# Optimization experiments

Measured on AMD Instinct MI355X. Metric: run time of the kernel, lower is better.

The kernel has to match this reference:

```python
import jax, jax.numpy as jnp
import numpy as np

D_MODEL = 1024
N_HEADS = 16
D_K = D_MODEL // N_HEADS


def setup_inputs() -> dict:
    key = jax.random.key(0)
    ks = jax.random.split(key, 11)
    B, S = 2, 2048
    scale = 1.0 / np.sqrt(D_MODEL)
    inp = {
        "Q_in": jax.random.normal(ks[0], (B, S, D_MODEL), jnp.float32),
        "K_in": jax.random.normal(ks[1], (B, S, D_MODEL), jnp.float32),
        "V_in": jax.random.normal(ks[2], (B, S, D_MODEL), jnp.float32),
        # torch nn.Linear convention: y = x @ W.T + b, W shape [out, in]
        "W_q": jax.random.normal(ks[3], (D_MODEL, D_MODEL), jnp.float32) * scale,
        "b_q": jax.random.normal(ks[4], (D_MODEL,), jnp.float32) * scale,
        "W_k": jax.random.normal(ks[5], (D_MODEL, D_MODEL), jnp.float32) * scale,
        "b_k": jax.random.normal(ks[6], (D_MODEL,), jnp.float32) * scale,
        "W_v": jax.random.normal(ks[7], (D_MODEL, D_MODEL), jnp.float32) * scale,
        "b_v": jax.random.normal(ks[8], (D_MODEL,), jnp.float32) * scale,
        "W_o": jax.random.normal(ks[9], (D_MODEL, D_MODEL), jnp.float32) * scale,
        "b_o": jax.random.normal(ks[10], (D_MODEL,), jnp.float32) * scale,
    }
    return inp


def reference(Q_in, K_in, V_in, W_q, b_q, W_k, b_k, W_v, b_v, W_o, b_o):
    B, S, _ = Q_in.shape

    def proj(x, W, b):
        # [B,S,D] -> [B,H,S,dk]
        y = x @ W.T + b
        return y.reshape(B, S, N_HEADS, D_K).transpose(0, 2, 1, 3)

    Q = proj(Q_in, W_q, b_q)
    K = proj(K_in, W_k, b_k)
    V = proj(V_in, W_v, b_v)

    scores = jnp.einsum("bhqd,bhkd->bhqk", Q, K) / jnp.sqrt(jnp.float32(D_K))
    attn_weights = jax.nn.softmax(scores, axis=-1)
    ctx = jnp.einsum("bhqk,bhkd->bhqd", attn_weights, V)
    ctx = ctx.transpose(0, 2, 1, 3).reshape(B, S, D_MODEL)
    output = ctx @ W_o.T + b_o
    return output, attn_weights
```

## Files before the change

kernel.cpp:

```cpp
#include <hip/hip_runtime.h>
#include <hip/hip_bf16.h>
#include <stdint.h>

typedef __attribute__((ext_vector_type(8))) short short8;
typedef __attribute__((ext_vector_type(4))) short short4v;
typedef __attribute__((ext_vector_type(4))) float f32x4;
typedef __attribute__((ext_vector_type(2))) float f32x2;

#define MFMA16x16x32(A, B, C) __builtin_amdgcn_mfma_f32_16x16x32_bf16((A), (B), (C), 0, 0, 0)

static constexpr int kS  = 2048;
static constexpr int kD  = 1024;
static constexpr int kDK = 64;

static constexpr size_t OFF_XQ  = 0;
static constexpr size_t OFF_XK  = 4194304;
static constexpr size_t OFF_XV  = 8388608;
static constexpr size_t OFF_W   = 12582912;
static constexpr size_t OFF_QP  = 16777216;
static constexpr size_t OFF_KP  = 20971520;
static constexpr size_t OFF_VT  = 25165824;
static constexpr size_t OFF_CTX = 29360128;

__device__ __forceinline__ short f2bf(float f) {
  __hip_bfloat16 h = __float2bfloat16(f);
  return *reinterpret_cast<short*>(&h);
}

__global__ __launch_bounds__(256) void cvt_kernel(
    const float* __restrict__ xq, const float* __restrict__ xk, const float* __restrict__ xv,
    const float* __restrict__ wq, const float* __restrict__ wk, const float* __restrict__ wv,
    const float* __restrict__ wo, __hip_bfloat16* __restrict__ dst)
{
  int g = blockIdx.x * 256 + threadIdx.x;
  const float* src;
  __hip_bfloat16* d;
  int rel;
  if (g < 3145728) {
    int seg = g >> 20; rel = g & 1048575;
    src = seg == 0 ? xq : (seg == 1 ? xk : xv);
    d = dst + (size_t)seg * 4194304;
  } else {
    int g2 = g - 3145728; int seg = g2 >> 18; rel = g2 & 262143;
    src = seg == 0 ? wq : (seg == 1 ? wk : (seg == 2 ? wv : wo));
    d = dst + OFF_W + (size_t)seg * 1048576;
  }
  float4 v = ((const float4*)src)[rel];
  short4v o;
  o.x = f2bf(v.x); o.y = f2bf(v.y); o.z = f2bf(v.z); o.w = f2bf(v.w);
  ((short4v*)d)[rel] = o;
}

__device__ __forceinline__ void stage_tile(short* lds, const __hip_bfloat16* g0, int t) {
  #pragma unroll
  for (int c = 0; c < 2; ++c) {
    const int e = t * 8 + c * 2048;
    const int row = e >> 5;
    const int kk = e & 31;
    __builtin_amdgcn_global_load_lds(
        (const __attribute__((address_space(1))) void*)(g0 + (size_t)row * kD + kk),
        (__attribute__((address_space(3))) void*)(lds + e), 16, 0, 0);
  }
}

__device__ __forceinline__ void gemm_main(const __hip_bfloat16* X, const __hip_bfloat16* W,
                                          short* As, short* Bs, f32x4 acc[4][4])
{
  const int t = threadIdx.x;
  const int lane = t & 63;
  const int wv = t >> 6;
  const int wr = wv >> 1, wc = wv & 1;
  const int fr = lane & 15;
  const int fc = (lane >> 4) * 8;
  for (int k0 = 0; k0 < kD; k0 += 32) {
    stage_tile(As, X + k0, t);
    stage_tile(Bs, W + k0, t);
    __syncthreads();
    short8 af[4], bfv[4];
    #pragma unroll
    for (int i = 0; i < 4; ++i) af[i]  = *(const short8*)&As[(wr * 64 + i * 16 + fr) * 32 + fc];
    #pragma unroll
    for (int i = 0; i < 4; ++i) bfv[i] = *(const short8*)&Bs[(wc * 64 + i * 16 + fr) * 32 + fc];
    #pragma unroll
    for (int i = 0; i < 4; ++i)
      #pragma unroll
      for (int j = 0; j < 4; ++j)
        acc[i][j] = MFMA16x16x32(af[i], bfv[j], acc[i][j]);
    __syncthreads();
  }
}

__global__ __launch_bounds__(256) void qkv_gemm(
    const __hip_bfloat16* __restrict__ Xq, const __hip_bfloat16* __restrict__ Xk,
    const __hip_bfloat16* __restrict__ Xv, const __hip_bfloat16* __restrict__ Wbase,
    const float* __restrict__ bq, const float* __restrict__ bk, const float* __restrict__ bv,
    __hip_bfloat16* __restrict__ Qp, __hip_bfloat16* __restrict__ Kp,
    __hip_bfloat16* __restrict__ Vt)
{
  __shared__ __align__(16) short As[128 * 32];
  __shared__ __align__(16) short Bs[128 * 32];
  const int z  = blockIdx.z;
  const int m0 = blockIdx.y * 128, n0 = blockIdx.x * 128;
  const __hip_bfloat16* X = (z == 0 ? Xq : (z == 1 ? Xk : Xv)) + (size_t)m0 * kD;
  const __hip_bfloat16* W = Wbase + (size_t)z * (kD * kD) + (size_t)n0 * kD;
  const float* bias = (z == 0 ? bq : (z == 1 ? bk : bv));
  f32x4 acc[4][4] = {};
  gemm_main(X, W, As, Bs, acc);

  const int lane = threadIdx.x & 63;
  const int wv = threadIdx.x >> 6;
  const int wr = wv >> 1, wc = wv & 1;
  short* dstQK = (short*)(z == 0 ? Qp : Kp);
  short* dstV  = (short*)Vt;
  #pragma unroll
  for (int i = 0; i < 4; ++i) {
    #pragma unroll
    for (int j = 0; j < 4; ++j) {
      #pragma unroll
      for (int r = 0; r < 4; ++r) {
        int m = m0 + wr * 64 + i * 16 + (lane >> 4) * 4 + r;
        int n = n0 + wc * 64 + j * 16 + (lane & 15);
        float y = acc[i][j][r] + bias[n];
        if (z == 0) y *= 0.125f;
        int b = m >> 11, sq = m & 2047, h = n >> 6, d = n & 63;
        if (z < 2)
          dstQK[((size_t)(b * 16 + h) * kS + sq) * kDK + d] = f2bf(y);
        else
          dstV[((size_t)(b * 16 + h) * kDK + d) * kS + sq] = f2bf(y);
      }
    }
  }
}

__global__ __launch_bounds__(256) void attn_pass1(
    const __hip_bfloat16* __restrict__ Qp, const __hip_bfloat16* __restrict__ Kp,
    const __hip_bfloat16* __restrict__ Vt, __hip_bfloat16* __restrict__ Ctx,
    float* __restrict__ rinvp)
{
  __shared__ __align__(16) short Ks[2][32][68];
  __shared__ __align__(16) short Vs[2][64][36];
  __shared__ __align__(16) short Ps[4][16][36];
  const int t = threadIdx.x;
  const int lane = t & 63;
  const int w = t >> 6;
  const int fr = lane & 15;
  const int g4 = lane >> 4;
  const int fc = g4 * 8;

  const int id  = blockIdx.x;
  const int swz = (id & 7) * 128 + (id >> 3);
  const int bh  = swz >> 5;
  const int q0  = (swz & 31) * 64 + w * 16;

  const __hip_bfloat16* Qh = Qp + (size_t)bh * kS * kDK;
  const __hip_bfloat16* Kh = Kp + (size_t)bh * kS * kDK;
  const __hip_bfloat16* Vh = Vt + (size_t)bh * kDK * kS;

  const short8 qf0 = *(const short8*)(Qh + (size_t)(q0 + fr) * kDK + fc);
  const short8 qf1 = *(const short8*)(Qh + (size_t)(q0 + fr) * kDK + 32 + fc);

  const int kr = t >> 3, kc = (t & 7) * 8;
  const int vr = t >> 2, vc = (t & 3) * 8;

  f32x4 ctxacc[4] = {};
  float ssumq = 0.f;

  short8 kA, vA, kB, vB;

#define LOAD_T(KREG, VREG, TI)                                                   \
  KREG = *(const short8*)(Kh + (size_t)((TI) * 32 + kr) * kDK + kc);             \
  VREG = *(const short8*)(Vh + (size_t)vr * kS + (TI) * 32 + vc);

#define STORE_T(KREG, VREG, BUF)                                                 \
  *(short8*)&Ks[BUF][kr][kc] = KREG;                                             \
  *(short8*)&Vs[BUF][vr][vc] = VREG;

#define COMPUTE_T(BUF)                                                           \
  {                                                                              \
    short8 k0a = *(const short8*)&Ks[BUF][fr][fc];                               \
    short8 k0b = *(const short8*)&Ks[BUF][fr][32 + fc];                          \
    short8 k1a = *(const short8*)&Ks[BUF][16 + fr][fc];                          \
    short8 k1b = *(const short8*)&Ks[BUF][16 + fr][32 + fc];                     \
    f32x4 s0 = {}; s0 = MFMA16x16x32(k0a, qf0, s0); s0 = MFMA16x16x32(k0b, qf1, s0); \
    f32x4 s1 = {}; s1 = MFMA16x16x32(k1a, qf0, s1); s1 = MFMA16x16x32(k1b, qf1, s1); \
    float e00 = __expf(s0[0]), e01 = __expf(s0[1]);                              \
    float e02 = __expf(s0[2]), e03 = __expf(s0[3]);                              \
    float e10 = __expf(s1[0]), e11 = __expf(s1[1]);                              \
    float e12 = __expf(s1[2]), e13 = __expf(s1[3]);                              \
    ssumq += (e00 + e01) + (e02 + e03) + (e10 + e11) + (e12 + e13);              \
    short4v p0, p1;                                                              \
    p0.x = f2bf(e00); p0.y = f2bf(e01); p0.z = f2bf(e02); p0.w = f2bf(e03);      \
    p1.x = f2bf(e10); p1.y = f2bf(e11); p1.z = f2bf(e12); p1.w = f2bf(e13);      \
    *(short4v*)&Ps[w][fr][g4 * 4]      = p0;                                     \
    *(short4v*)&Ps[w][fr][16 + g4 * 4] = p1;                                     \
    short8 pf = *(const short8*)&Ps[w][fr][fc];                                  \
    _Pragma("unroll")                                                            \
    for (int dc = 0; dc < 4; ++dc) {                                             \
      short8 vf = *(const short8*)&Vs[BUF][dc * 16 + fr][fc];                    \
      ctxacc[dc] = MFMA16x16x32(pf, vf, ctxacc[dc]);                             \
    }                                                                            \
  }

  LOAD_T(kA, vA, 0);
  STORE_T(kA, vA, 0);
  LOAD_T(kB, vB, 1);
  __syncthreads();

  for (int i = 0; i < 64; i += 2) {
    COMPUTE_T(0);
    STORE_T(kB, vB, 1);
    if (i + 2 < 64) { LOAD_T(kA, vA, i + 2); }
    __syncthreads();
    COMPUTE_T(1);
    if (i + 2 < 64) { STORE_T(kA, vA, 0); }
    if (i + 3 < 64) { LOAD_T(kB, vB, i + 3); }
    __syncthreads();
  }

  float s = ssumq;
  s += __shfl_xor(s, 16);
  s += __shfl_xor(s, 32);
  const float rvq = 1.0f / s;
  if (g4 == 0) rinvp[(size_t)bh * kS + q0 + fr] = rvq;

  float rinv4[4];
  #pragma unroll
  for (int j = 0; j < 4; ++j) rinv4[j] = __shfl(rvq, g4 * 4 + j, 16);

  const int b = bh >> 4, h = bh & 15;
  #pragma unroll
  for (int dc = 0; dc < 4; ++dc) {
    #pragma unroll
    for (int j = 0; j < 4; ++j) {
      int r = g4 * 4 + j;
      float v = ctxacc[dc][j] * rinv4[j];
      ((short*)Ctx)[((size_t)(b * kS + q0 + r)) * kD + h * kDK + dc * 16 + fr] = f2bf(v);
    }
  }
#undef LOAD_T
#undef STORE_T
#undef COMPUTE_T
}

__global__ __launch_bounds__(256) void fused_tail(
    const __hip_bfloat16* __restrict__ Ctx, const __hip_bfloat16* __restrict__ Wo,
    const float* __restrict__ bo, float* __restrict__ out,
    const __hip_bfloat16* __restrict__ Qp, const __hip_bfloat16* __restrict__ Kp,
    const float* __restrict__ rinvp, float* __restrict__ Aw)
{
  __shared__ __align__(16) short As[128 * 32];
  __shared__ __align__(16) short Bs[128 * 32];
  const int t = threadIdx.x;
  const int lane = t & 63;
  const int w = t >> 6;
  const int fr = lane & 15;
  const int g4 = lane >> 4;
  const int fc = g4 * 8;

  if (blockIdx.x < 256) {
    const int m0 = (blockIdx.x >> 3) * 128, n0 = (blockIdx.x & 7) * 128;
    f32x4 acc[4][4] = {};
    gemm_main(Ctx + (size_t)m0 * kD, Wo + (size_t)n0 * kD, As, Bs, acc);
    const int wr = w >> 1, wc = w & 1;
    #pragma unroll
    for (int i = 0; i < 4; ++i) {
      #pragma unroll
      for (int j = 0; j < 4; ++j) {
        #pragma unroll
        for (int r = 0; r < 4; ++r) {
          int m = m0 + wr * 64 + i * 16 + g4 * 4 + r;
          int n = n0 + wc * 64 + j * 16 + fr;
          __builtin_nontemporal_store(acc[i][j][r] + bo[n], &out[(size_t)m * kD + n]);
        }
      }
    }
    return;
  }

  const int id  = blockIdx.x - 256;
  const int swz = (id & 7) * 512 + (id >> 3);
  const int bh  = swz >> 7;
  const int ksg = (swz >> 5) & 3;
  const int q0  = (swz & 31) * 64 + w * 16;
  const int k0  = ksg * 512;

  const __hip_bfloat16* Qh = Qp + (size_t)bh * kS * kDK;
  const __hip_bfloat16* Kh = Kp + (size_t)bh * kS * kDK;

  const short8 qf0 = *(const short8*)(Qh + (size_t)(q0 + fr) * kDK + fc);
  const short8 qf1 = *(const short8*)(Qh + (size_t)(q0 + fr) * kDK + 32 + fc);

  const float rvq = rinvp[(size_t)bh * kS + q0 + fr];
  float* aw = Aw + ((size_t)bh * kS + q0 + fr) * kS;

  short8 ka[8], kb[8];

#define LOADK(ARR, KT_)                                                          \
  _Pragma("unroll")                                                              \
  for (int c = 0; c < 4; ++c) {                                                  \
    ARR[2 * c]     = *(const short8*)(Kh + (size_t)((KT_) + c * 16 + fr) * kDK + fc);      \
    ARR[2 * c + 1] = *(const short8*)(Kh + (size_t)((KT_) + c * 16 + fr) * kDK + 32 + fc); \
  }

#define CSTORE(ARR, KT_)                                                         \
  _Pragma("unroll")                                                              \
  for (int c = 0; c < 4; ++c) {                                                  \
    f32x4 st = {};                                                               \
    st = MFMA16x16x32(ARR[2 * c], qf0, st);                                      \
    st = MFMA16x16x32(ARR[2 * c + 1], qf1, st);                                  \
    f32x4 v;                                                                     \
    _Pragma("unroll")                                                            \
    for (int j = 0; j < 4; ++j) v[j] = __expf(st[j]) * rvq;                      \
    __builtin_nontemporal_store(v, (f32x4*)(aw + (KT_) + c * 16 + g4 * 4));      \
  }

  LOADK(ka, k0);
  for (int kt = k0; kt < k0 + 512; kt += 128) {
    LOADK(kb, kt + 64);
    CSTORE(ka, kt);
    if (kt + 128 < k0 + 512) { LOADK(ka, kt + 128); }
    CSTORE(kb, kt + 64);
  }
#undef LOADK
#undef CSTORE
}

extern "C" void kernel_launch(void* const* d_in, const int* in_sizes, int n_in,
                              void* d_out, int out_size, void* d_ws, size_t ws_size,
                              hipStream_t stream) {
  (void)in_sizes; (void)n_in; (void)out_size; (void)ws_size;
  const float* Qin = (const float*)d_in[0];
  const float* Kin = (const float*)d_in[1];
  const float* Vin = (const float*)d_in[2];
  const float* Wq  = (const float*)d_in[3];
  const float* bq  = (const float*)d_in[4];
  const float* Wk  = (const float*)d_in[5];
  const float* bk  = (const float*)d_in[6];
  const float* Wv  = (const float*)d_in[7];
  const float* bv  = (const float*)d_in[8];
  const float* Wo  = (const float*)d_in[9];
  const float* bo  = (const float*)d_in[10];
  __hip_bfloat16* ws = (__hip_bfloat16*)d_ws;
  float* out = (float*)d_out;
  float* rinvp = (float*)(ws + OFF_XQ);

  cvt_kernel<<<16384, 256, 0, stream>>>(Qin, Kin, Vin, Wq, Wk, Wv, Wo, ws);
  qkv_gemm<<<dim3(8, 32, 3), 256, 0, stream>>>(
      ws + OFF_XQ, ws + OFF_XK, ws + OFF_XV, ws + OFF_W, bq, bk, bv,
      ws + OFF_QP, ws + OFF_KP, ws + OFF_VT);
  attn_pass1<<<1024, 256, 0, stream>>>(
      ws + OFF_QP, ws + OFF_KP, ws + OFF_VT, ws + OFF_CTX, rinvp);
  fused_tail<<<4352, 256, 0, stream>>>(
      ws + OFF_CTX, ws + OFF_W + 3 * 1048576, bo, out,
      ws + OFF_QP, ws + OFF_KP, rinvp, out + 4194304);
}
```

Before: 291.7 us.

## Split attention key range across two blocks and add a reduction kernel

The attention pass now splits each head's 2048 keys into two halves handled by separate blocks, doubling the grid from 1024 to 2048 blocks. Each block writes unnormalized partial context in bf16 and its partial row sums. A new reduce kernel adds the two partials, normalizes them, and writes the final context and inverse sums. The aim is more parallelism and better CU occupancy on MI355X, at the cost of an extra launch, extra global traffic, and bf16 rounding of the partials.

Result: no change. 295.2 us (+1.2%).

```diff
diff --git a/kernel.cpp b/kernel.cpp
--- a/kernel.cpp
+++ b/kernel.cpp
@@ -25,6 +25,12 @@
 __device__ __forceinline__ short f2bf(float f) {
   __hip_bfloat16 h = __float2bfloat16(f);
   return *reinterpret_cast<short*>(&h);
+}
+
+__device__ __forceinline__ float bf2f(short s) {
+  union { unsigned u; float f; } cv;
+  cv.u = ((unsigned)(unsigned short)s) << 16;
+  return cv.f;
 }
 
 __global__ __launch_bounds__(256) void cvt_kernel(
@@ -132,10 +138,10 @@
   }
 }
 
-__global__ __launch_bounds__(256) void attn_pass1(
+__global__ __launch_bounds__(256) void attn_pass1_split(
     const __hip_bfloat16* __restrict__ Qp, const __hip_bfloat16* __restrict__ Kp,
-    const __hip_bfloat16* __restrict__ Vt, __hip_bfloat16* __restrict__ Ctx,
-    float* __restrict__ rinvp)
+    const __hip_bfloat16* __restrict__ Vt, __hip_bfloat16* __restrict__ ctxp,
+    float* __restrict__ partp)
 {
   __shared__ __align__(16) short Ks[2][32][68];
   __shared__ __align__(16) short Vs[2][64][36];
@@ -148,9 +154,11 @@
   const int fc = g4 * 8;
 
   const int id  = blockIdx.x;
-  const int swz = (id & 7) * 128 + (id >> 3);
-  const int bh  = swz >> 5;
+  const int swz = (id & 7) * 256 + (id >> 3);
+  const int bh  = swz >> 6;
+  const int ksg = (swz >> 5) & 1;
   const int q0  = (swz & 31) * 64 + w * 16;
+  const int kbase = ksg << 10;
 
   const __hip_bfloat16* Qh = Qp + (size_t)bh * kS * kDK;
   const __hip_bfloat16* Kh = Kp + (size_t)bh * kS * kDK;
@@ -168,8 +176,8 @@
   short8 kA, vA, kB, vB;
 
 #define LOAD_T(KREG, VREG, TI)                                                   \
-  KREG = *(const short8*)(Kh + (size_t)((TI) * 32 + kr) * kDK + kc);             \
-  VREG = *(const short8*)(Vh + (size_t)vr * kS + (TI) * 32 + vc);
+  KREG = *(const short8*)(Kh + (size_t)(kbase + (TI) * 32 + kr) * kDK + kc);     \
+  VREG = *(const short8*)(Vh + (size_t)vr * kS + kbase + (TI) * 32 + vc);
 
 #define STORE_T(KREG, VREG, BUF)                                                 \
   *(short8*)&Ks[BUF][kr][kc] = KREG;                                             \
@@ -206,40 +214,61 @@
   LOAD_T(kB, vB, 1);
   __syncthreads();
 
-  for (int i = 0; i < 64; i += 2) {
+  for (int i = 0; i < 32; i += 2) {
     COMPUTE_T(0);
     STORE_T(kB, vB, 1);
-    if (i + 2 < 64) { LOAD_T(kA, vA, i + 2); }
+    if (i + 2 < 32) { LOAD_T(kA, vA, i + 2); }
     __syncthreads();
     COMPUTE_T(1);
-    if (i + 2 < 64) { STORE_T(kA, vA, 0); }
-    if (i + 3 < 64) { LOAD_T(kB, vB, i + 3); }
+    if (i + 2 < 32) { STORE_T(kA, vA, 0); }
+    if (i + 3 < 32) { LOAD_T(kB, vB, i + 3); }
     __syncthreads();
   }
 
   float s = ssumq;
   s += __shfl_xor(s, 16);
   s += __shfl_xor(s, 32);
-  const float rvq = 1.0f / s;
-  if (g4 == 0) rinvp[(size_t)bh * kS + q0 + fr] = rvq;
-
-  float rinv4[4];
-  #pragma unroll
-  for (int j = 0; j < 4; ++j) rinv4[j] = __shfl(rvq, g4 * 4 + j, 16);
-
-  const int b = bh >> 4, h = bh & 15;
+  if (g4 == 0) partp[((size_t)bh * 2 + ksg) * kS + q0 + fr] = s;
+
+  short* cp = (short*)ctxp;
   #pragma unroll
   for (int dc = 0; dc < 4; ++dc) {
     #pragma unroll
     for (int j = 0; j < 4; ++j) {
       int r = g4 * 4 + j;
-      float v = ctxacc[dc][j] * rinv4[j];
-      ((short*)Ctx)[((size_t)(b * kS + q0 + r)) * kD + h * kDK + dc * 16 + fr] = f2bf(v);
+      cp[(((size_t)bh * 2 + ksg) * kS + q0 + r) * kDK + dc * 16 + fr] = f2bf(ctxacc[dc][j]);
     }
   }
 #undef LOAD_T
 #undef STORE_T
 #undef COMPUTE_T
+}
+
+__global__ __launch_bounds__(256) void reduce_ctx(
+    const __hip_bfloat16* __restrict__ ctxp, const float* __restrict__ partp,
+    __hip_bfloat16* __restrict__ Ctx, float* __restrict__ rinvp)
+{
+  const int idx = blockIdx.x * 256 + threadIdx.x;
+  const int d16 = idx & 15;
+  const int q   = (idx >> 4) & 2047;
+  const int bh  = idx >> 15;
+
+  const float rv = 1.0f / (partp[(size_t)bh * 2 * kS + q] +
+                           partp[((size_t)bh * 2 + 1) * kS + q]);
+
+  const short* c0 = (const short*)ctxp + ((size_t)bh * 2 * kS + q) * kDK + d16 * 4;
+  const short* c1 = (const short*)ctxp + (((size_t)bh * 2 + 1) * kS + q) * kDK + d16 * 4;
+  short4v a = *(const short4v*)c0;
+  short4v b2 = *(const short4v*)c1;
+  short4v o;
+  #pragma unroll
+  for (int j = 0; j < 4; ++j) {
+    float v = (bf2f(a[j]) + bf2f(b2[j])) * rv;
+    o[j] = f2bf(v);
+  }
+  const int b = bh >> 4, h = bh & 15;
+  *(short4v*)((short*)Ctx + ((size_t)(b * kS + q)) * kD + h * kDK + d16 * 4) = o;
+  if (d16 == 0) rinvp[(size_t)bh * kS + q] = rv;
 }
 
 __global__ __launch_bounds__(256) void fused_tail(
@@ -342,14 +371,17 @@
   const float* bo  = (const float*)d_in[10];
   __hip_bfloat16* ws = (__hip_bfloat16*)d_ws;
   float* out = (float*)d_out;
-  float* rinvp = (float*)(ws + OFF_XQ);
+  float* partp = (float*)(ws + OFF_XQ);
+  float* rinvp = partp + 131072;
+  __hip_bfloat16* ctxp = ws + OFF_XK;
 
   cvt_kernel<<<16384, 256, 0, stream>>>(Qin, Kin, Vin, Wq, Wk, Wv, Wo, ws);
   qkv_gemm<<<dim3(8, 32, 3), 256, 0, stream>>>(
       ws + OFF_XQ, ws + OFF_XK, ws + OFF_XV, ws + OFF_W, bq, bk, bv,
       ws + OFF_QP, ws + OFF_KP, ws + OFF_VT);
-  attn_pass1<<<1024, 256, 0, stream>>>(
-      ws + OFF_QP, ws + OFF_KP, ws + OFF_VT, ws + OFF_CTX, rinvp);
+  attn_pass1_split<<<2048, 256, 0, stream>>>(
+      ws + OFF_QP, ws + OFF_KP, ws + OFF_VT, ctxp, partp);
+  reduce_ctx<<<4096, 256, 0, stream>>>(ctxp, partp, ws + OFF_CTX, rinvp);
   fused_tail<<<4352, 256, 0, stream>>>(
       ws + OFF_CTX, ws + OFF_W + 3 * 1048576, bo, out,
       ws + OFF_QP, ws + OFF_KP, rinvp, out + 4194304);
```
